# Optimization experiments

Hardware: AMD Instinct MI355X
Metric: run time of the kernel (lower is better)

## Reference

```python
import jax, jax.numpy as jnp
import numpy as np

B, S, D, H = 8, 2048, 1024, 16
HD = D // H  # head_dim = 64


def setup_inputs() -> dict:
    key = jax.random.key(0)
    ks = jax.random.split(key, 10)
    s = 0.02
    return {
        "x": jax.random.normal(ks[0], (B, S, D), jnp.float32),
        "mask": jnp.zeros((B, 1, S), jnp.float32),
        "Wq": jax.random.normal(ks[1], (D, D), jnp.float32) * s,
        "bq": jnp.zeros((D,), jnp.float32),
        "Wk": jax.random.normal(ks[2], (D, D), jnp.float32) * s,
        "bk": jnp.zeros((D,), jnp.float32),
        "Wv": jax.random.normal(ks[3], (D, D), jnp.float32) * s,
        "bv": jnp.zeros((D,), jnp.float32),
        "wa": jax.random.normal(ks[4], (HD, 1), jnp.float32) * s,
        "ba": jnp.zeros((1,), jnp.float32),
        "wb": jax.random.normal(ks[5], (HD, 1), jnp.float32) * s,
        "bb": jnp.zeros((1,), jnp.float32),
        "Wu": jax.random.normal(ks[6], (HD, HD), jnp.float32) * s,
        "bu": jnp.zeros((HD,), jnp.float32),
        "Wo": jax.random.normal(ks[7], (D, D), jnp.float32) * s,
        "bo": jnp.zeros((D,), jnp.float32),
        "gamma": jnp.ones((D,), jnp.float32),
        "beta_ln": jnp.zeros((D,), jnp.float32),
    }


def _split_heads(t):
    # [B,S,D] -> [B,H,S,HD]
    return t.reshape(B, S, H, HD).transpose(0, 2, 1, 3)


def reference(x, mask, Wq, bq, Wk, bk, Wv, bv, wa, ba, wb, bb, Wu, bu, Wo, bo, gamma, beta_ln):
    scale = 1.0 / jnp.sqrt(jnp.float32(HD))
    q = _split_heads(x @ Wq + bq)  # [B,H,S,HD]
    k = _split_heads(x @ Wk + bk)
    v = _split_heads(x @ Wv + bv)

    # additive attention over queries -> global query vector per head
    alphascore = (jnp.squeeze(q @ wa, -1) + ba[0]) * scale + mask  # [B,H,S]
    alphaw = jax.nn.softmax(alphascore, axis=-1)
    q_av = jnp.einsum('bhs,bhsd->bhd', alphaw, q)

    p = k * q_av[:, :, None, :]  # gated keys [B,H,S,HD]
    betascore = (jnp.squeeze(p @ wb, -1) + bb[0]) * scale + mask
    betaw = jax.nn.softmax(betascore, axis=-1)
    p_av = jnp.einsum('bhs,bhsd->bhd', betaw, p)

    u = v * p_av[:, :, None, :]  # gated values
    r = u @ Wu + bu  # [B,H,S,HD]
    newr = (r + q).transpose(0, 2, 1, 3).reshape(B, S, D)
    attn_out = newr @ Wo + bo

    h = x + attn_out
    mu = jnp.mean(h, axis=-1, keepdims=True)
    var = jnp.mean(jnp.square(h - mu), axis=-1, keepdims=True)
    return (h - mu) * jax.lax.rsqrt(var + 1e-6) * gamma + beta_ln
```

## Files before the change

kernel.cpp:

```cpp
#include <hip/hip_runtime.h>
#include <cstdint>

#define BB 8
#define SS 2048
#define DD 1024
#define HH 16
#define HDIM 64
#define MTOT (BB*SS)
#define QKVW 2048

typedef __attribute__((ext_vector_type(8))) __bf16 bf16x8;
typedef __attribute__((ext_vector_type(4))) float f32x4;

#define AS1(p) ((const __attribute__((address_space(1))) void*)(p))
#define AS3(p) ((__attribute__((address_space(3))) void*)(p))

__device__ __forceinline__ float bf2f(uint16_t u){
  return __uint_as_float(((uint32_t)u) << 16);
}
__device__ __forceinline__ uint16_t f2bf(float f){
  uint32_t u = __float_as_uint(f);
  return (uint16_t)((u + 0x7fffu + ((u >> 16) & 1u)) >> 16);
}

__global__ __launch_bounds__(256)
void k_prep(const float* __restrict__ x,
            const float* __restrict__ Wq, const float* __restrict__ Wk,
            const float* __restrict__ Wv, const float* __restrict__ Wo,
            const float* __restrict__ bq, const float* __restrict__ bv,
            uint16_t* __restrict__ xb, uint16_t* __restrict__ Wt,
            uint16_t* __restrict__ Wkt, uint16_t* __restrict__ WoT,
            float* __restrict__ bqv)
{
  __shared__ float t[32][33];
  const int blk = blockIdx.x, tid = threadIdx.x;
  if (blk < 2048){
    const int n4 = MTOT*DD/4;
    for (int i = blk*256 + tid; i < n4; i += 2048*256){
      float4 v = reinterpret_cast<const float4*>(x)[i];
      ushort4 o;
      o.x = f2bf(v.x); o.y = f2bf(v.y); o.z = f2bf(v.z); o.w = f2bf(v.w);
      reinterpret_cast<ushort4*>(xb)[i] = o;
    }
  } else if (blk < 6144){
    const int zb = blk - 2048;
    const int z = zb >> 10, rem = zb & 1023;
    const int by = rem >> 5, bx = rem & 31;
    const float* src = (z==0)?Wq:(z==1)?Wv:(z==2)?Wk:Wo;
    uint16_t* dst = (z==0)?Wt:(z==1)?(Wt + 1024*1024):(z==2)?Wkt:WoT;
    const int k0 = by*32, n0 = bx*32;
    const int tx = tid & 31, ty = tid >> 5;
    #pragma unroll
    for (int r = 0; r < 4; ++r)
      t[ty + r*8][tx] = src[(size_t)(k0 + ty + r*8)*1024 + n0 + tx];
    __syncthreads();
    #pragma unroll
    for (int r = 0; r < 4; ++r)
      dst[(size_t)(n0 + ty + r*8)*1024 + k0 + tx] = f2bf(t[tx][ty + r*8]);
  } else {
    const int i = (blk - 6144)*256 + tid;
    if (i < QKVW)
      bqv[i] = (i < 1024) ? bq[i] : bv[i-1024];
  }
}

#define BARRIER __builtin_amdgcn_s_barrier()

#define READA(BUF, MH) { \
  const uint16_t* _sl = lds + ((BUF)*4 + (MH))*8192; \
  _Pragma("unroll") \
  for (int f = 0; f < 4; ++f) \
    _Pragma("unroll") \
    for (int ks = 0; ks < 2; ++ks) \
      a[f][ks] = *(const bf16x8*)(_sl + (wm*64 + f*16 + l15)*64 + (((ks*4 + l4) ^ l7)<<3)); \
}

#define READB(BUF, NH, BV) { \
  const uint16_t* _sl = lds + ((BUF)*4 + 2 + (NH))*8192; \
  _Pragma("unroll") \
  for (int j = 0; j < 2; ++j) \
    _Pragma("unroll") \
    for (int ks = 0; ks < 2; ++ks) \
      BV[j][ks] = *(const bf16x8*)(_sl + (wn*32 + j*16 + l15)*64 + (((ks*4 + l4) ^ l7)<<3)); \
}

#define MMA(MH, NH, BV) { \
  __builtin_amdgcn_s_setprio(1); \
  _Pragma("unroll") \
  for (int ks = 0; ks < 2; ++ks) \
    _Pragma("unroll") \
    for (int f = 0; f < 4; ++f) \
      _Pragma("unroll") \
      for (int j = 0; j < 2; ++j) \
        acc[(MH)*4+f][(NH)*2+j] = __builtin_amdgcn_mfma_f32_16x16x32_bf16(a[f][ks], BV[j][ks], acc[(MH)*4+f][(NH)*2+j], 0, 0, 0); \
  __builtin_amdgcn_s_setprio(0); }

#define STAGEA(T, H) { \
  char* _d = (char*)lds + ((((T)&1)*4 + (H))*16384) + wave*1024; \
  _Pragma("unroll") \
  for (int l = 0; l < 2; ++l) \
    __builtin_amdgcn_global_load_lds(AS1(pA + (l*131072 + (H)*65536 + (T)*64)), AS3(_d + l*8192), 16, 0, 0); \
}

#define STAGEB(T, H) { \
  char* _d = (char*)lds + ((((T)&1)*4 + 2 + (H))*16384) + wave*1024; \
  _Pragma("unroll") \
  for (int l = 0; l < 2; ++l) \
    __builtin_amdgcn_global_load_lds(AS1(pB + (l*131072 + (H)*32768 + (T)*64)), AS3(_d + l*8192), 16, 0, 0); \
}

template<int EPI, int NB_T>
__global__ __launch_bounds__(512)
void k_gemm256(const uint16_t* __restrict__ A, const uint16_t* __restrict__ Bt,
               const float* __restrict__ bias, const uint16_t* __restrict__ resid16,
               uint16_t* __restrict__ Cout,
               const float* __restrict__ waP, const float* __restrict__ baP,
               const float* __restrict__ maskP,
               float* __restrict__ cpartA, float* __restrict__ dpartA)
{
  constexpr int N = NB_T * 256;
  __shared__ uint16_t lds[8 * 8192];
  const int tid = threadIdx.x;
  const int lane = tid & 63, wave = tid >> 6;
  const int wm = wave >> 2, wn = wave & 3;
  const int l15 = lane & 15, l4 = lane >> 4, l7 = lane & 7;

  const int nwg = gridDim.x, cpx = nwg >> 3, bid = blockIdx.x;
  const int wg = (bid & 7) * cpx + (bid >> 3);
  const int m0 = (wg / NB_T) << 8, n0 = (wg % NB_T) << 8;

  const int colbase = (((tid & 7) ^ ((tid >> 3) & 7)) << 3);
  const uint16_t* pA = A  + (size_t)(m0 + (tid >> 3)) * 1024 + colbase;
  const uint16_t* pB = Bt + (size_t)(n0 + ((tid >> 8) << 6) + ((tid >> 3) & 31)) * 1024 + colbase;

  f32x4 acc[8][4] = {};
  bf16x8 a[4][2], b0[2][2], b1[2][2];

  STAGEA(0,0); STAGEB(0,1); STAGEA(0,1); STAGEB(0,0);
  STAGEA(1,0); STAGEB(1,1); STAGEA(1,1);
  asm volatile("s_waitcnt vmcnt(6)" ::: "memory");
  BARRIER;

  #pragma unroll
  for (int I = 0; I < 7; ++I){
    const int e = 2*I;
    READA(0,0); READB(0,0,b0); STAGEB(e+1, 0);
    BARRIER; MMA(0,0,b0); BARRIER;
    READB(0,1,b1); STAGEA(e+2, 0);
    BARRIER; MMA(0,1,b1); BARRIER;
    READA(0,1); STAGEB(e+2, 1);
    BARRIER; MMA(1,1,b1); BARRIER;
    STAGEA(e+2, 1);
    asm volatile("s_waitcnt vmcnt(6)" ::: "memory");
    BARRIER; MMA(1,0,b0); BARRIER;
    READA(1,0); READB(1,0,b0); STAGEB(e+2, 0);
    BARRIER; MMA(0,0,b0); BARRIER;
    READB(1,1,b1); STAGEA(e+3, 0);
    BARRIER; MMA(0,1,b1); BARRIER;
    READA(1,1); STAGEB(e+3, 1);
    BARRIER; MMA(1,1,b1); BARRIER;
    STAGEA(e+3, 1);
    asm volatile("s_waitcnt vmcnt(6)" ::: "memory");
    BARRIER; MMA(1,0,b0); BARRIER;
  }

  {
    READA(0,0); READB(0,0,b0); STAGEB(15, 0);
    BARRIER; MMA(0,0,b0); BARRIER;
    READB(0,1,b1);
    BARRIER; MMA(0,1,b1); BARRIER;
    READA(0,1);
    BARRIER; MMA(1,1,b1); BARRIER;
    asm volatile("s_waitcnt vmcnt(0)" ::: "memory");
    BARRIER; MMA(1,0,b0); BARRIER;
    READA(1,0); READB(1,0,b0);
    BARRIER; MMA(0,0,b0); BARRIER;
    READB(1,1,b1);
    BARRIER; MMA(0,1,b1); BARRIER;
    READA(1,1);
    BARRIER; MMA(1,1,b1); BARRIER;
    MMA(1,0,b0);
  }

  #pragma unroll
  for (int mh = 0; mh < 2; ++mh)
  #pragma unroll
  for (int f = 0; f < 4; ++f)
  #pragma unroll
  for (int nh = 0; nh < 2; ++nh)
  #pragma unroll
  for (int j = 0; j < 2; ++j){
    const int gcol = n0 + wn*64 + nh*32 + j*16 + l15;
    const float bi = bias[gcol];
    const int rbase = m0 + wm*128 + mh*64 + f*16 + l4*4;
    #pragma unroll
    for (int rr = 0; rr < 4; ++rr){
      const size_t idx = (size_t)(rbase + rr)*N + gcol;
      float v = acc[mh*4+f][nh*2+j][rr] + bi;
      if (EPI == 1) v += bf2f(resid16[idx]);
      Cout[idx] = f2bf(v);
    }
  }

  if (EPI == 0 && n0 < 1024){
    const int hg = (n0 >> 6) + wn;
    const float bav = baP[0];
    float bcol[2][2], wv[2][2];
    #pragma unroll
    for (int nh = 0; nh < 2; ++nh)
    #pragma unroll
    for (int j = 0; j < 2; ++j){
      const int c = nh*32 + j*16 + l15;
      bcol[nh][j] = bias[n0 + wn*64 + c];
      wv[nh][j]   = waP[c];
    }
    float colacc[2][2] = {{0.f,0.f},{0.f,0.f}};
    float esum = 0.f;
    #pragma unroll
    for (int mh = 0; mh < 2; ++mh)
    #pragma unroll
    for (int f = 0; f < 4; ++f)
    #pragma unroll
    for (int rr = 0; rr < 4; ++rr){
      float qv[2][2];
      float p = 0.f;
      #pragma unroll
      for (int nh = 0; nh < 2; ++nh)
      #pragma unroll
      for (int j = 0; j < 2; ++j){
        qv[nh][j] = acc[mh*4+f][nh*2+j][rr] + bcol[nh][j];
        p += qv[nh][j] * wv[nh][j];
      }
      p += __shfl_xor(p, 1); p += __shfl_xor(p, 2);
      p += __shfl_xor(p, 4); p += __shfl_xor(p, 8);
      const int grow = m0 + wm*128 + mh*64 + f*16 + l4*4 + rr;
      const float E = __expf((p + bav)*0.125f + maskP[grow]);
      esum += E;
      #pragma unroll
      for (int nh = 0; nh < 2; ++nh)
      #pragma unroll
      for (int j = 0; j < 2; ++j)
        colacc[nh][j] += E * qv[nh][j];
    }
    const int rb = (m0 >> 7) + wm;
    #pragma unroll
    for (int nh = 0; nh < 2; ++nh)
    #pragma unroll
    for (int j = 0; j < 2; ++j){
      float v = colacc[nh][j];
      v += __shfl_xor(v, 16); v += __shfl_xor(v, 32);
      if (l4 == 0)
        cpartA[(size_t)rb*1024 + n0 + wn*64 + nh*32 + j*16 + l15] = v;
    }
    esum += __shfl_xor(esum, 16); esum += __shfl_xor(esum, 32);
    if (lane == 0) dpartA[rb*16 + hg] = esum;
  }
}

__global__ __launch_bounds__(256)
void k_mergefold(const float* __restrict__ cpartA, const float* __restrict__ dpartA,
                 const float* __restrict__ wb, const uint16_t* __restrict__ Wkt,
                 const float* __restrict__ bk, const float* __restrict__ bbP,
                 float* __restrict__ qavB, uint16_t* __restrict__ pBb,
                 float* __restrict__ csB)
{
  __shared__ float wl[64];
  __shared__ float redc[64];
  const int bh = blockIdx.x, b = bh >> 4, h = bh & 15;
  const int tid = threadIdx.x;
  if (tid < 64){
    float s = 0.f;
    #pragma unroll
    for (int rb = 0; rb < 16; ++rb)
      s += cpartA[(size_t)(b*16 + rb)*1024 + h*64 + tid];
    float d = 0.f;
    #pragma unroll
    for (int rb = 0; rb < 16; ++rb)
      d += dpartA[(b*16 + rb)*16 + h];
    const float qv = s / d;
    qavB[b*1024 + h*64 + tid] = qv;
    wl[tid] = qv * wb[tid];
  }
  __syncthreads();
  const int k0 = tid*4;
  float a0 = 0.f, a1 = 0.f, a2 = 0.f, a3 = 0.f;
  for (int d2 = 0; d2 < 64; ++d2){
    const float w = wl[d2];
    const ushort4 r = *(const ushort4*)(Wkt + (size_t)(h*64 + d2)*1024 + k0);
    a0 += bf2f(r.x)*w; a1 += bf2f(r.y)*w; a2 += bf2f(r.z)*w; a3 += bf2f(r.w)*w;
  }
  uint16_t* dst = pBb + (size_t)bh*1024 + k0;
  dst[0] = f2bf(a0); dst[1] = f2bf(a1); dst[2] = f2bf(a2); dst[3] = f2bf(a3);
  if (tid < 64) redc[tid] = bk[h*64 + tid] * wl[tid];
  __syncthreads();
  if (tid == 0){
    float s = 0.f;
    for (int i = 0; i < 64; ++i) s += redc[i];
    csB[bh] = s + bbP[0];
  }
}

__global__ __launch_bounds__(512)
void k_scoreXsum(const uint16_t* __restrict__ xb, const uint16_t* __restrict__ pBb,
                 const float* __restrict__ csB, const float* __restrict__ mask,
                 float* __restrict__ xwp, float* __restrict__ dpartB)
{
  __shared__ float el[64][16];
  __shared__ float sred[4][16];
  __shared__ float csl[16];
  const int blk = blockIdx.x, tid = threadIdx.x;
  const int b = blk >> 5;
  const int wave = tid >> 6, lane = tid & 63;
  const int l15 = lane & 15, l4 = lane >> 4;
  if (tid < 16) csl[tid] = csB[b*16 + tid];
  __syncthreads();
  const int row0 = blk*64;

  if (wave < 4){
    const int rw = row0 + wave*16;
    const uint16_t* pa = xb  + (size_t)(rw + l15)*1024 + l4*8;
    const uint16_t* pb = pBb + (size_t)(b*16 + l15)*1024 + l4*8;
    f32x4 acc = {};
    #pragma unroll
    for (int kk = 0; kk < 32; ++kk){
      const bf16x8 af = *(const bf16x8*)(pa + kk*32);
      const bf16x8 bf = *(const bf16x8*)(pb + kk*32);
      acc = __builtin_amdgcn_mfma_f32_16x16x32_bf16(af, bf, acc, 0, 0, 0);
    }
    float es = 0.f;
    #pragma unroll
    for (int r = 0; r < 4; ++r){
      const int rloc = wave*16 + l4*4 + r;
      const float E = __expf((acc[r] + csl[l15])*0.125f + mask[row0 + rloc]);
      el[rloc][l15] = E;
      es += E;
    }
    es += __shfl_xor(es, 16); es += __shfl_xor(es, 32);
    if (l4 == 0) sred[wave][l15] = es;
  }
  __syncthreads();
  if (tid < 16)
    dpartB[blk*16 + tid] = sred[0][tid] + sred[1][tid] + sred[2][tid] + sred[3][tid];

  const int c0 = tid*2;
  float acc0[16], acc1[16];
  #pragma unroll
  for (int h = 0; h < 16; ++h){ acc0[h] = 0.f; acc1[h] = 0.f; }
  for (int r = 0; r < 64; ++r){
    const uint32_t xv = *(const uint32_t*)(xb + (size_t)(row0 + r)*1024 + c0);
    const float x0 = __uint_as_float(xv << 16);
    const float x1 = __uint_as_float(xv & 0xffff0000u);
    const float4 e0 = *(const float4*)(&el[r][0]);
    const float4 e1 = *(const float4*)(&el[r][4]);
    const float4 e2 = *(const float4*)(&el[r][8]);
    const float4 e3 = *(const float4*)(&el[r][12]);
    acc0[0]  += x0*e0.x; acc1[0]  += x1*e0.x;
    acc0[1]  += x0*e0.y; acc1[1]  += x1*e0.y;
    acc0[2]  += x0*e0.z; acc1[2]  += x1*e0.z;
    acc0[3]  += x0*e0.w; acc1[3]  += x1*e0.w;
    acc0[4]  += x0*e1.x; acc1[4]  += x1*e1.x;
    acc0[5]  += x0*e1.y; acc1[5]  += x1*e1.y;
    acc0[6]  += x0*e1.z; acc1[6]  += x1*e1.z;
    acc0[7]  += x0*e1.w; acc1[7]  += x1*e1.w;
    acc0[8]  += x0*e2.x; acc1[8]  += x1*e2.x;
    acc0[9]  += x0*e2.y; acc1[9]  += x1*e2.y;
    acc0[10] += x0*e2.z; acc1[10] += x1*e2.z;
    acc0[11] += x0*e2.w; acc1[11] += x1*e2.w;
    acc0[12] += x0*e3.x; acc1[12] += x1*e3.x;
    acc0[13] += x0*e3.y; acc1[13] += x1*e3.y;
    acc0[14] += x0*e3.z; acc1[14] += x1*e3.z;
    acc0[15] += x0*e3.w; acc1[15] += x1*e3.w;
  }
  float* dst = xwp + (size_t)blk*16*1024;
  #pragma unroll
  for (int h = 0; h < 16; ++h)
    *(float2*)(dst + h*1024 + c0) = (float2){acc0[h], acc1[h]};
}

__global__ __launch_bounds__(512)
void k_finalB(const float* __restrict__ xwp, const float* __restrict__ dpartB,
              const float* __restrict__ qavB, const uint16_t* __restrict__ Wkt,
              const float* __restrict__ bk, const float* __restrict__ Wu,
              uint16_t* __restrict__ WuPT)
{
  __shared__ float xwl[1024];
  __shared__ float kvl[64];
  __shared__ float pavl[64];
  __shared__ float dsh;
  const int bh = blockIdx.x, b = bh >> 4, h = bh & 15;
  const int tid = threadIdx.x;
  #pragma unroll
  for (int i = 0; i < 2; ++i){
    const int idx = i*512 + tid;
    float s = 0.f;
    #pragma unroll
    for (int rc = 0; rc < 32; ++rc)
      s += xwp[((size_t)(b*32 + rc)*16 + h)*1024 + idx];
    xwl[idx] = s;
  }
  if (tid < 32){
    float d = dpartB[(b*32 + tid)*16 + h];
    d += __shfl_xor(d, 1); d += __shfl_xor(d, 2); d += __shfl_xor(d, 4);
    d += __shfl_xor(d, 8); d += __shfl_xor(d, 16);
    if (tid == 0) dsh = d;
  }
  __syncthreads();
  const int d = tid >> 3, q = tid & 7;
  const uint16_t* wrow = Wkt + (size_t)(h*64 + d)*1024 + q*128;
  const float* xwq = xwl + q*128;
  float s = 0.f;
  #pragma unroll
  for (int i = 0; i < 16; ++i){
    const bf16x8 v = *(const bf16x8*)(wrow + i*8);
    #pragma unroll
    for (int e = 0; e < 8; ++e) s += (float)v[e]*xwq[i*8+e];
  }
  s += __shfl_xor(s, 1); s += __shfl_xor(s, 2); s += __shfl_xor(s, 4);
  if (q == 0) kvl[d] = s;
  __syncthreads();
  if (tid < 64)
    pavl[tid] = qavB[b*1024 + h*64 + tid] * (kvl[tid]/dsh + bk[h*64 + tid]);
  __syncthreads();
  uint16_t* dst = WuPT + (size_t)bh*4096;
  for (int idx = tid; idx < 4096; idx += 512){
    const int i = idx & 63, jcol = idx >> 6;
    dst[idx] = f2bf(pavl[i]*Wu[i*64 + jcol]);
  }
}

__global__ __launch_bounds__(256)
void k_newr(const uint16_t* __restrict__ qkv, const uint16_t* __restrict__ WuPT,
            const float* __restrict__ bu, uint16_t* __restrict__ newr)
{
  const int bh = blockIdx.x >> 3, st = blockIdx.x & 7;
  const int b = bh >> 4, h = bh & 15;
  const int tid = threadIdx.x, wave = tid >> 6, lane = tid & 63;
  const int l15 = lane & 15, l4 = lane >> 4;
  const int s0 = st*256 + wave*64;
  const uint16_t* vb = qkv + 1024 + h*64;
  const uint16_t* wt = WuPT + (size_t)bh*4096;

  f32x4 acc[4][4] = {};
  #pragma unroll
  for (int ks = 0; ks < 2; ++ks){
    bf16x8 bfr[4];
    #pragma unroll
    for (int n = 0; n < 4; ++n)
      bfr[n] = *(const bf16x8*)(wt + (n*16 + l15)*64 + ks*32 + l4*8);
    #pragma unroll
    for (int m = 0; m < 4; ++m){
      const int s = s0 + m*16 + l15;
      bf16x8 af = *(const bf16x8*)(vb + (size_t)(b*SS + s)*QKVW + ks*32 + l4*8);
      #pragma unroll
      for (int n = 0; n < 4; ++n)
        acc[m][n] = __builtin_amdgcn_mfma_f32_16x16x32_bf16(af, bfr[n], acc[m][n], 0, 0, 0);
    }
  }
  #pragma unroll
  for (int n = 0; n < 4; ++n){
    const int j = n*16 + l15;
    const float bj = bu[j];
    #pragma unroll
    for (int m = 0; m < 4; ++m){
      #pragma unroll
      for (int r = 0; r < 4; ++r){
        const int s = s0 + m*16 + l4*4 + r;
        const size_t qidx = (size_t)(b*SS + s)*QKVW + h*64 + j;
        const float q = bf2f(qkv[qidx]);
        newr[(size_t)(b*SS + s)*DD + h*64 + j] = f2bf(acc[m][n][r] + bj + q);
      }
    }
  }
}

__global__ __launch_bounds__(256)
void k_ln(const uint16_t* __restrict__ h16, const float* __restrict__ gamma,
          const float* __restrict__ beta, float* __restrict__ out)
{
  __shared__ float r1[256], r2[256];
  const int row = blockIdx.x, tid = threadIdx.x;
  const ushort4 hv = ((const ushort4*)(h16 + (size_t)row*DD))[tid];
  float v0 = bf2f(hv.x), v1 = bf2f(hv.y), v2 = bf2f(hv.z), v3 = bf2f(hv.w);
  float s  = v0 + v1 + v2 + v3;
  float ss = v0*v0 + v1*v1 + v2*v2 + v3*v3;
  r1[tid] = s; r2[tid] = ss; __syncthreads();
  for (int off = 128; off > 0; off >>= 1){
    if (tid < off){ r1[tid] += r1[tid+off]; r2[tid] += r2[tid+off]; }
    __syncthreads();
  }
  const float mu  = r1[0]*(1.f/1024.f);
  const float var = r2[0]*(1.f/1024.f) - mu*mu;
  const float inv = rsqrtf(var + 1e-6f);
  const float4 g  = ((const float4*)gamma)[tid];
  const float4 be = ((const float4*)beta)[tid];
  float4 o;
  o.x = (v0-mu)*inv*g.x + be.x;
  o.y = (v1-mu)*inv*g.y + be.y;
  o.z = (v2-mu)*inv*g.z + be.z;
  o.w = (v3-mu)*inv*g.w + be.w;
  ((float4*)(out + (size_t)row*DD))[tid] = o;
}

extern "C" void kernel_launch(void* const* d_in, const int* in_sizes, int n_in,
                              void* d_out, int out_size, void* d_ws, size_t ws_size,
                              hipStream_t stream) {
  const float* x    = (const float*)d_in[0];
  const float* mask = (const float*)d_in[1];
  const float* Wq   = (const float*)d_in[2];
  const float* bq   = (const float*)d_in[3];
  const float* Wk   = (const float*)d_in[4];
  const float* bk   = (const float*)d_in[5];
  const float* Wv   = (const float*)d_in[6];
  const float* bv   = (const float*)d_in[7];
  const float* wa   = (const float*)d_in[8];
  const float* ba   = (const float*)d_in[9];
  const float* wb   = (const float*)d_in[10];
  const float* bb   = (const float*)d_in[11];
  const float* Wu   = (const float*)d_in[12];
  const float* bu   = (const float*)d_in[13];
  const float* Wo   = (const float*)d_in[14];
  const float* bo   = (const float*)d_in[15];
  const float* gamma= (const float*)d_in[16];
  const float* beta = (const float*)d_in[17];
  float* out = (float*)d_out;

  char* ws = (char*)d_ws;
  const size_t MB = 1ull << 20;
  uint16_t* xb    = (uint16_t*)(ws);
  uint16_t* Wt    = (uint16_t*)(ws + 32*MB);
  uint16_t* Wkt   = (uint16_t*)(ws + 36*MB);
  uint16_t* WoT   = (uint16_t*)(ws + 38*MB);
  float*    bqv   = (float*)   (ws + 40*MB);
  uint16_t* WuPT  = (uint16_t*)(ws + 41*MB);
  uint16_t* qkv   = (uint16_t*)(ws + 42*MB);
  uint16_t* hbuf16= (uint16_t*)(ws + 42*MB);
  float* cpartA = (float*)(ws + 110*MB);
  float* dpartA = (float*)(ws + 111*MB);
  float* qavB   = (float*)(ws + 112*MB);
  uint16_t* pBb = (uint16_t*)(ws + 114*MB);
  float* csB    = (float*)(ws + 115*MB);
  float* dpartB = (float*)(ws + 118*MB);
  float* xwp    = (float*)(ws + 119*MB);
  uint16_t* newr= (uint16_t*)(ws + 138*MB);

  k_prep<<<6156, 256, 0, stream>>>(x, Wq, Wk, Wv, Wo, bq, bv, xb, Wt, Wkt, WoT, bqv);

  k_gemm256<0,8><<<(MTOT/256)*(QKVW/256), 512, 0, stream>>>(
      xb, Wt, bqv, nullptr, qkv, wa, ba, mask, cpartA, dpartA);

  k_mergefold<<<128, 256, 0, stream>>>(cpartA, dpartA, wb, Wkt, bk, bb, qavB, pBb, csB);
  k_scoreXsum<<<256, 512, 0, stream>>>(xb, pBb, csB, mask, xwp, dpartB);
  k_finalB<<<128, 512, 0, stream>>>(xwp, dpartB, qavB, Wkt, bk, Wu, WuPT);

  k_newr<<<BB*HH*8, 256, 0, stream>>>(qkv, WuPT, bu, newr);
  k_gemm256<1,4><<<(MTOT/256)*(DD/256), 512, 0, stream>>>(
      newr, WoT, bo, xb, hbuf16, nullptr, nullptr, nullptr, nullptr, nullptr);
  k_ln<<<MTOT, 256, 0, stream>>>(hbuf16, gamma, beta, out);
}
```

Before: 216.9 us.

## Fuse LayerNorm row statistics into output GEMM epilogue and split k_newr finer

The output-projection GEMM epilogue now computes per-row partial sums and sums of squares of the residual-added values. It reduces them across waves through LDS and writes per-256-column partials to a small buffer. The LayerNorm kernel then reads these eight partials instead of running its own shared-memory tree reduction with many barriers. Separately, k_newr is launched with twice as many blocks, each handling half as many rows, to raise parallelism. The costs are an extra barrier and LDS traffic in the GEMM epilogue, and statistics computed from unrounded fp32 values rather than the stored bf16.

```diff
diff --git a/kernel.cpp b/kernel.cpp
--- a/kernel.cpp
+++ b/kernel.cpp
@@ -116,7 +116,8 @@
                uint16_t* __restrict__ Cout,
                const float* __restrict__ waP, const float* __restrict__ baP,
                const float* __restrict__ maskP,
-               float* __restrict__ cpartA, float* __restrict__ dpartA)
+               float* __restrict__ cpartA, float* __restrict__ dpartA,
+               float* __restrict__ lnpart)
 {
   constexpr int N = NB_T * 256;
   __shared__ uint16_t lds[8 * 8192];
@@ -182,78 +183,124 @@
     MMA(1,0,b0);
   }
 
-  #pragma unroll
-  for (int mh = 0; mh < 2; ++mh)
-  #pragma unroll
-  for (int f = 0; f < 4; ++f)
-  #pragma unroll
-  for (int nh = 0; nh < 2; ++nh)
-  #pragma unroll
-  for (int j = 0; j < 2; ++j){
-    const int gcol = n0 + wn*64 + nh*32 + j*16 + l15;
-    const float bi = bias[gcol];
-    const int rbase = m0 + wm*128 + mh*64 + f*16 + l4*4;
+  if (EPI == 0){
+    #pragma unroll
+    for (int mh = 0; mh < 2; ++mh)
+    #pragma unroll
+    for (int f = 0; f < 4; ++f)
+    #pragma unroll
+    for (int nh = 0; nh < 2; ++nh)
+    #pragma unroll
+    for (int j = 0; j < 2; ++j){
+      const int gcol = n0 + wn*64 + nh*32 + j*16 + l15;
+      const float bi = bias[gcol];
+      const int rbase = m0 + wm*128 + mh*64 + f*16 + l4*4;
+      #pragma unroll
+      for (int rr = 0; rr < 4; ++rr){
+        const size_t idx = (size_t)(rbase + rr)*N + gcol;
+        Cout[idx] = f2bf(acc[mh*4+f][nh*2+j][rr] + bi);
+      }
+    }
+    if (n0 < 1024){
+      const int hg = (n0 >> 6) + wn;
+      const float bav = baP[0];
+      float bcol[2][2], wv[2][2];
+      #pragma unroll
+      for (int nh = 0; nh < 2; ++nh)
+      #pragma unroll
+      for (int j = 0; j < 2; ++j){
+        const int c = nh*32 + j*16 + l15;
+        bcol[nh][j] = bias[n0 + wn*64 + c];
+        wv[nh][j]   = waP[c];
+      }
+      float colacc[2][2] = {{0.f,0.f},{0.f,0.f}};
+      float esum = 0.f;
+      #pragma unroll
+      for (int mh = 0; mh < 2; ++mh)
+      #pragma unroll
+      for (int f = 0; f < 4; ++f)
+      #pragma unroll
+      for (int rr = 0; rr < 4; ++rr){
+        float qv[2][2];
+        float p = 0.f;
+        #pragma unroll
+        for (int nh = 0; nh < 2; ++nh)
+        #pragma unroll
+        for (int j = 0; j < 2; ++j){
+          qv[nh][j] = acc[mh*4+f][nh*2+j][rr] + bcol[nh][j];
+          p += qv[nh][j] * wv[nh][j];
+        }
+        p += __shfl_xor(p, 1); p += __shfl_xor(p, 2);
+        p += __shfl_xor(p, 4); p += __shfl_xor(p, 8);
+        const int grow = m0 + wm*128 + mh*64 + f*16 + l4*4 + rr;
+        const float E = __expf((p + bav)*0.125f + maskP[grow]);
+        esum += E;
+        #pragma unroll
+        for (int nh = 0; nh < 2; ++nh)
+        #pragma unroll
+        for (int j = 0; j < 2; ++j)
+          colacc[nh][j] += E * qv[nh][j];
+      }
+      const int rb = (m0 >> 7) + wm;
+      #pragma unroll
+      for (int nh = 0; nh < 2; ++nh)
+      #pragma unroll
+      for (int j = 0; j < 2; ++j){
+        float v = colacc[nh][j];
+        v += __shfl_xor(v, 16); v += __shfl_xor(v, 32);
+        if (l4 == 0)
+          cpartA[(size_t)rb*1024 + n0 + wn*64 + nh*32 + j*16 + l15] = v;
+      }
+      esum += __shfl_xor(esum, 16); esum += __shfl_xor(esum, 32);
+      if (lane == 0) dpartA[rb*16 + hg] = esum;
+    }
+  } else {
+    float* lnw = (float*)lds;
+    __syncthreads();
+    float bcol[2][2];
+    #pragma unroll
+    for (int nh = 0; nh < 2; ++nh)
+    #pragma unroll
+    for (int j = 0; j < 2; ++j)
+      bcol[nh][j] = bias[n0 + wn*64 + nh*32 + j*16 + l15];
+    #pragma unroll
+    for (int mh = 0; mh < 2; ++mh)
+    #pragma unroll
+    for (int f = 0; f < 4; ++f)
     #pragma unroll
     for (int rr = 0; rr < 4; ++rr){
-      const size_t idx = (size_t)(rbase + rr)*N + gcol;
-      float v = acc[mh*4+f][nh*2+j][rr] + bi;
-      if (EPI == 1) v += bf2f(resid16[idx]);
-      Cout[idx] = f2bf(v);
-    }
-  }
-
-  if (EPI == 0 && n0 < 1024){
-    const int hg = (n0 >> 6) + wn;
-    const float bav = baP[0];
-    float bcol[2][2], wv[2][2];
-    #pragma unroll
-    for (int nh = 0; nh < 2; ++nh)
-    #pragma unroll
-    for (int j = 0; j < 2; ++j){
-      const int c = nh*32 + j*16 + l15;
-      bcol[nh][j] = bias[n0 + wn*64 + c];
-      wv[nh][j]   = waP[c];
-    }
-    float colacc[2][2] = {{0.f,0.f},{0.f,0.f}};
-    float esum = 0.f;
-    #pragma unroll
-    for (int mh = 0; mh < 2; ++mh)
-    #pragma unroll
-    for (int f = 0; f < 4; ++f)
-    #pragma unroll
-    for (int rr = 0; rr < 4; ++rr){
-      float qv[2][2];
-      float p = 0.f;
+      const int row_local = wm*128 + mh*64 + f*16 + l4*4 + rr;
+      const int grow = m0 + row_local;
+      float rs = 0.f, rss = 0.f;
       #pragma unroll
       for (int nh = 0; nh < 2; ++nh)
       #pragma unroll
       for (int j = 0; j < 2; ++j){
-        qv[nh][j] = acc[mh*4+f][nh*2+j][rr] + bcol[nh][j];
-        p += qv[nh][j] * wv[nh][j];
+        const int gcol = n0 + wn*64 + nh*32 + j*16 + l15;
+        const size_t idx = (size_t)grow*N + gcol;
+        float v = acc[mh*4+f][nh*2+j][rr] + bcol[nh][j] + bf2f(resid16[idx]);
+        Cout[idx] = f2bf(v);
+        rs += v; rss += v*v;
       }
-      p += __shfl_xor(p, 1); p += __shfl_xor(p, 2);
-      p += __shfl_xor(p, 4); p += __shfl_xor(p, 8);
-      const int grow = m0 + wm*128 + mh*64 + f*16 + l4*4 + rr;
-      const float E = __expf((p + bav)*0.125f + maskP[grow]);
-      esum += E;
-      #pragma unroll
-      for (int nh = 0; nh < 2; ++nh)
-      #pragma unroll
-      for (int j = 0; j < 2; ++j)
-        colacc[nh][j] += E * qv[nh][j];
-    }
-    const int rb = (m0 >> 7) + wm;
-    #pragma unroll
-    for (int nh = 0; nh < 2; ++nh)
-    #pragma unroll
-    for (int j = 0; j < 2; ++j){
-      float v = colacc[nh][j];
-      v += __shfl_xor(v, 16); v += __shfl_xor(v, 32);
-      if (l4 == 0)
-        cpartA[(size_t)rb*1024 + n0 + wn*64 + nh*32 + j*16 + l15] = v;
-    }
-    esum += __shfl_xor(esum, 16); esum += __shfl_xor(esum, 32);
-    if (lane == 0) dpartA[rb*16 + hg] = esum;
+      rs  += __shfl_xor(rs, 1);  rs  += __shfl_xor(rs, 2);
+      rs  += __shfl_xor(rs, 4);  rs  += __shfl_xor(rs, 8);
+      rss += __shfl_xor(rss, 1); rss += __shfl_xor(rss, 2);
+      rss += __shfl_xor(rss, 4); rss += __shfl_xor(rss, 8);
+      if (l15 == 0){
+        lnw[(wn*256 + row_local)*2 + 0] = rs;
+        lnw[(wn*256 + row_local)*2 + 1] = rss;
+      }
+    }
+    __syncthreads();
+    if (tid < 256){
+      const float s  = lnw[(0*256+tid)*2] + lnw[(1*256+tid)*2]
+                     + lnw[(2*256+tid)*2] + lnw[(3*256+tid)*2];
+      const float ss = lnw[(0*256+tid)*2+1] + lnw[(1*256+tid)*2+1]
+                     + lnw[(2*256+tid)*2+1] + lnw[(3*256+tid)*2+1];
+      const int grow = m0 + tid;
+      lnpart[(size_t)grow*8 + (n0 >> 8)*2 + 0] = s;
+      lnpart[(size_t)grow*8 + (n0 >> 8)*2 + 1] = ss;
+    }
   }
 }
 
@@ -432,15 +479,15 @@
 void k_newr(const uint16_t* __restrict__ qkv, const uint16_t* __restrict__ WuPT,
             const float* __restrict__ bu, uint16_t* __restrict__ newr)
 {
-  const int bh = blockIdx.x >> 3, st = blockIdx.x & 7;
+  const int bh = blockIdx.x >> 4, st = blockIdx.x & 15;
   const int b = bh >> 4, h = bh & 15;
   const int tid = threadIdx.x, wave = tid >> 6, lane = tid & 63;
   const int l15 = lane & 15, l4 = lane >> 4;
-  const int s0 = st*256 + wave*64;
+  const int s0 = st*128 + wave*32;
   const uint16_t* vb = qkv + 1024 + h*64;
   const uint16_t* wt = WuPT + (size_t)bh*4096;
 
-  f32x4 acc[4][4] = {};
+  f32x4 acc[2][4] = {};
   #pragma unroll
   for (int ks = 0; ks < 2; ++ks){
     bf16x8 bfr[4];
@@ -448,7 +495,7 @@
     for (int n = 0; n < 4; ++n)
       bfr[n] = *(const bf16x8*)(wt + (n*16 + l15)*64 + ks*32 + l4*8);
     #pragma unroll
-    for (int m = 0; m < 4; ++m){
+    for (int m = 0; m < 2; ++m){
       const int s = s0 + m*16 + l15;
       bf16x8 af = *(const bf16x8*)(vb + (size_t)(b*SS + s)*QKVW + ks*32 + l4*8);
       #pragma unroll
@@ -461,7 +508,7 @@
     const int j = n*16 + l15;
     const float bj = bu[j];
     #pragma unroll
-    for (int m = 0; m < 4; ++m){
+    for (int m = 0; m < 2; ++m){
       #pragma unroll
       for (int r = 0; r < 4; ++r){
         const int s = s0 + m*16 + l4*4 + r;
@@ -474,22 +521,20 @@
 }
 
 __global__ __launch_bounds__(256)
-void k_ln(const uint16_t* __restrict__ h16, const float* __restrict__ gamma,
-          const float* __restrict__ beta, float* __restrict__ out)
+void k_ln(const uint16_t* __restrict__ h16, const float* __restrict__ lnpart,
+          const float* __restrict__ gamma, const float* __restrict__ beta,
+          float* __restrict__ out)
 {
-  __shared__ float r1[256], r2[256];
+  __shared__ float pp[8];
   const int row = blockIdx.x, tid = threadIdx.x;
+  if (tid < 8) pp[tid] = lnpart[(size_t)row*8 + tid];
   const ushort4 hv = ((const ushort4*)(h16 + (size_t)row*DD))[tid];
-  float v0 = bf2f(hv.x), v1 = bf2f(hv.y), v2 = bf2f(hv.z), v3 = bf2f(hv.w);
-  float s  = v0 + v1 + v2 + v3;
-  float ss = v0*v0 + v1*v1 + v2*v2 + v3*v3;
-  r1[tid] = s; r2[tid] = ss; __syncthreads();
-  for (int off = 128; off > 0; off >>= 1){
-    if (tid < off){ r1[tid] += r1[tid+off]; r2[tid] += r2[tid+off]; }
-    __syncthreads();
-  }
-  const float mu  = r1[0]*(1.f/1024.f);
-  const float var = r2[0]*(1.f/1024.f) - mu*mu;
+  const float v0 = bf2f(hv.x), v1 = bf2f(hv.y), v2 = bf2f(hv.z), v3 = bf2f(hv.w);
+  __syncthreads();
+  const float s  = pp[0] + pp[2] + pp[4] + pp[6];
+  const float ss = pp[1] + pp[3] + pp[5] + pp[7];
+  const float mu  = s*(1.f/1024.f);
+  const float var = ss*(1.f/1024.f) - mu*mu;
   const float inv = rsqrtf(var + 1e-6f);
   const float4 g  = ((const float4*)gamma)[tid];
   const float4 be = ((const float4*)beta)[tid];
@@ -541,19 +586,20 @@
   float* csB    = (float*)(ws + 115*MB);
   float* dpartB = (float*)(ws + 118*MB);
   float* xwp    = (float*)(ws + 119*MB);
+  float* lnpart = (float*)(ws + 136*MB);
   uint16_t* newr= (uint16_t*)(ws + 138*MB);
 
   k_prep<<<6156, 256, 0, stream>>>(x, Wq, Wk, Wv, Wo, bq, bv, xb, Wt, Wkt, WoT, bqv);
 
   k_gemm256<0,8><<<(MTOT/256)*(QKVW/256), 512, 0, stream>>>(
-      xb, Wt, bqv, nullptr, qkv, wa, ba, mask, cpartA, dpartA);
+      xb, Wt, bqv, nullptr, qkv, wa, ba, mask, cpartA, dpartA, nullptr);
 
   k_mergefold<<<128, 256, 0, stream>>>(cpartA, dpartA, wb, Wkt, bk, bb, qavB, pBb, csB);
   k_scoreXsum<<<256, 512, 0, stream>>>(xb, pBb, csB, mask, xwp, dpartB);
   k_finalB<<<128, 512, 0, stream>>>(xwp, dpartB, qavB, Wkt, bk, Wu, WuPT);
 
-  k_newr<<<BB*HH*8, 256, 0, stream>>>(qkv, WuPT, bu, newr);
+  k_newr<<<BB*HH*16, 256, 0, stream>>>(qkv, WuPT, bu, newr);
   k_gemm256<1,4><<<(MTOT/256)*(DD/256), 512, 0, stream>>>(
-      newr, WoT, bo, xb, hbuf16, nullptr, nullptr, nullptr, nullptr, nullptr);
-  k_ln<<<MTOT, 256, 0, stream>>>(hbuf16, gamma, beta, out);
-}
+      newr, WoT, bo, xb, hbuf16, nullptr, nullptr, nullptr, nullptr, nullptr, lnpart);
+  k_ln<<<MTOT, 256, 0, stream>>>(hbuf16, lnpart, gamma, beta, out);
+}
```

New measurement: 223.2 us. 1.03x slower.
